# Optimization experiments

Measured on AMD Instinct MI355X. Metric: run time of the kernel, lower is better.

The kernel has to match this reference:

```python
import jax, jax.numpy as jnp
import numpy as np

# Detect.__init__ defaults from the source
TOP_K = 5000
CONF_THRESH = 0.01
NMS_THRESH = 0.3
VAR0, VAR1 = 0.1, 0.2   # variance = [0.1, 0.2]
NUM_CLASSES = 2

B = 16
IMAGE = 1280
FMAPS = [320, 160, 80, 40, 20, 10]          # image / steps [4,8,16,32,64,128]
MIN_SIZES = [16, 32, 64, 128, 256, 512]
AR = 1.5                                     # aspect_ratios = [[1.5]] * 6


def make_priors():
    """Vectorized PriorBox.forward: 1 prior per location (max_sizes=[], single AR)."""
    chunks = []
    for f, ms in zip(FMAPS, MIN_SIZES):
        c = (np.arange(f, dtype=np.float32) + 0.5) / f
        cy, cx = np.meshgrid(c, c, indexing='ij')
        s = ms / float(IMAGE)
        w = np.full_like(cx, s / np.sqrt(AR))   # s_k / sqrt(ar)
        h = np.full_like(cx, s * np.sqrt(AR))   # s_k * sqrt(ar)
        chunks.append(np.stack([cx, cy, w, h], -1).reshape(-1, 4))
    pr = np.concatenate(chunks, 0).clip(0.0, 1.0)   # clip=True
    return jnp.asarray(pr, jnp.float32)             # [136500, 4]


def setup_inputs() -> dict:
    key = jax.random.key(0)
    k1, k2 = jax.random.split(key)
    P = sum(f * f for f in FMAPS)   # 136500
    loc_data = 0.5 * jax.random.normal(k1, (B, P, 4), jnp.float32)
    conf_data = jax.random.uniform(k2, (B * P, NUM_CLASSES), jnp.float32)  # post-softmax probs
    prior_data = make_priors()
    return {"loc_data": loc_data, "conf_data": conf_data, "prior_data": prior_data}


def _decode(loc, priors):
    # SSD box decode with variances [0.1, 0.2]; loc, priors: [P,4]
    cxcy = priors[:, :2] + loc[:, :2] * VAR0 * priors[:, 2:]
    wh = priors[:, 2:] * jnp.exp(loc[:, 2:] * VAR1)
    xy1 = cxcy - wh * 0.5
    xy2 = xy1 + wh
    return jnp.concatenate([xy1, xy2], axis=-1)   # [P,4] x1y1x2y2


def _greedy_keep(boxes, valid):
    # Greedy NMS over score-sorted candidates. boxes [K,4], valid [K] bool.
    # Indices/keep decisions are discrete -> computed on stop_gradient'd boxes.
    b = jax.lax.stop_gradient(boxes)
    x1, y1, x2, y2 = b[:, 0], b[:, 1], b[:, 2], b[:, 3]
    area = (x2 - x1) * (y2 - y1)
    idxs = jnp.arange(b.shape[0])

    def body(keep, i):
        iw = jnp.maximum(jnp.minimum(x2, x2[i]) - jnp.maximum(x1, x1[i]), 0.0)
        ih = jnp.maximum(jnp.minimum(y2, y2[i]) - jnp.maximum(y1, y1[i]), 0.0)
        inter = iw * ih
        iou = inter / (area + area[i] - inter)
        suppress = keep[i] & (iou > NMS_THRESH) & (idxs > i)
        return keep & ~suppress, None

    keep, _ = jax.lax.scan(body, valid, idxs)
    return keep


def _detect_one(loc_i, conf_cl, priors):
    # loc_i [P,4]; conf_cl [P] = class-1 scores; returns [TOP_K, 5] (score, x1,y1,x2,y2)
    boxes = _decode(loc_i, priors)
    masked = jnp.where(conf_cl > CONF_THRESH, conf_cl, -1.0)   # c_mask gating
    order = jnp.argsort(-jax.lax.stop_gradient(masked))[:TOP_K]  # scores.sort, top_k cap
    s = masked[order]
    b = boxes[order]
    valid = s > CONF_THRESH
    keep = _greedy_keep(b, valid)
    # scatter kept (score, box) rows, in descending-score order, into dense output
    rank = jnp.cumsum(keep) - 1
    row = jnp.where(keep, rank, TOP_K)            # dropped rows -> scratch slot
    vals = jnp.concatenate([s[:, None], b], axis=1)
    vals = jnp.where(keep[:, None], vals, 0.0)
    out = jnp.zeros((TOP_K + 1, 5), jnp.float32).at[row].set(vals)
    return out[:TOP_K]


def reference(loc_data, conf_data, prior_data):
    num = loc_data.shape[0]
    P = prior_data.shape[0]
    conf_preds = conf_data.reshape(num, P, NUM_CLASSES).transpose(0, 2, 1)  # [B,2,P]
    cls1 = jax.vmap(_detect_one, in_axes=(0, 0, None))(loc_data, conf_preds[:, 1, :], prior_data)
    bg = jnp.zeros_like(cls1)                     # background class row stays zero
    output = jnp.stack([bg, cls1], axis=1)        # [B, 2, TOP_K, 5]
    # NOTE: the original's final `flt[(rank < top_k)...].fill_(0)` fills a boolean-indexed
    # COPY in torch, so it is a no-op on `output`; we faithfully return output unchanged.
    return output
```

## Files before the change

kernel.cpp:

```cpp
#include <hip/hip_runtime.h>
#include <math.h>

#pragma clang fp contract(off)

#define PNUM 136500
#define HPNUM 68250
#define BNUM 16
#define TOPK 5000
#define CAP 8192
#define NB2 1024
#define B2BASE 0xBC00u
#define NWORDS 79
#define NW32 158
#define GSTRIDE 32
#define CAPE 65536
#define ELDS 10240
#define NXB 128
#define BSTRIDE 5120
#define EBUF 3072

#define OFF_SC    ((size_t)0)
#define OFF_X1    (OFF_SC + 320000)
#define OFF_Y1    (OFF_X1 + 320000)
#define OFF_X2    (OFF_Y1 + 320000)
#define OFF_Y2    (OFF_X2 + 320000)
#define OFF_AREA  (OFF_Y2 + 320000)
#define OFF_HIST  ((size_t)1920000)
#define OFF_CUT   (OFF_HIST + 65536)
#define OFF_SBASE (OFF_CUT + 64)
#define OFF_GBCUR (OFF_SBASE + 65536)
#define OFF_KEYS  (OFF_GBCUR + 1048576)
#define OFF_ECNT  (OFF_KEYS + 1048576)
#define OFF_EDGE  (OFF_ECNT + 2048)
#define OFF_GRP   (OFF_EDGE + 4194304)
#define OFF_BOFS  (OFF_GRP)
#define OFF_SIDX  (OFF_GRP + 16384)
#define OFF_SBX1  (OFF_SIDX + 327680)
#define OFF_SBX2  (OFF_SBX1 + 327680)
#define OFF_SBY1  (OFF_SBX2 + 327680)
#define OFF_SBY2  (OFF_SBY1 + 327680)
#define OFF_SBAR  (OFF_SBY2 + 327680)

__device__ __forceinline__ unsigned f2ord(float f) {
    unsigned u = __float_as_uint(f);
    return (u & 0x80000000u) ? ~u : (u | 0x80000000u);
}
__device__ __forceinline__ float ord2f(unsigned o) {
    unsigned u = (o & 0x80000000u) ? (o ^ 0x80000000u) : ~o;
    return __uint_as_float(u);
}
__device__ __forceinline__ int bucketOf(float x) {
    int b = (int)((x + 0.6f) * 71.111115f);
    return (b < 0) ? 0 : ((b > 127) ? 127 : b);
}

__global__ void __launch_bounds__(256) k_hist(const float* __restrict__ conf,
                                              unsigned* __restrict__ hist) {
    __shared__ unsigned lh[NB2];
    int img = blockIdx.y;
    for (int i = threadIdx.x; i < NB2; i += 256) lh[i] = 0;
    __syncthreads();
    const float4* src = (const float4*)(conf + (size_t)img * PNUM * 2);
    int stride = gridDim.x * 256;
    for (int q = blockIdx.x * 256 + threadIdx.x; q < HPNUM; q += stride) {
        float4 v = src[q];
        if (v.y > 0.01f) atomicAdd(&lh[(f2ord(v.y) >> 16) - B2BASE], 1u);
        if (v.w > 0.01f) atomicAdd(&lh[(f2ord(v.w) >> 16) - B2BASE], 1u);
    }
    __syncthreads();
    unsigned* h = hist + (size_t)img * NB2;
    for (int i = threadIdx.x; i < NB2; i += 256) {
        unsigned c = lh[i];
        if (c) atomicAdd(&h[i], c);
    }
}

__global__ void __launch_bounds__(256) k_cutoff2(const unsigned* __restrict__ hist,
                                                 unsigned* __restrict__ cut,
                                                 unsigned* __restrict__ sbase) {
    __shared__ unsigned csum[256], suf[256];
    int img = blockIdx.x;
    int t = threadIdx.x;
    const unsigned* h = hist + (size_t)img * NB2;
    unsigned h0 = h[t * 4], h1 = h[t * 4 + 1], h2 = h[t * 4 + 2], h3 = h[t * 4 + 3];
    csum[t] = h0 + h1 + h2 + h3;
    __syncthreads();
    if (t == 0) {
        unsigned a = 0;
        for (int g = 255; g >= 0; --g) { unsigned c = csum[g]; suf[g] = a; a += c; }
        unsigned acc = 0, before = 0;
        int c = -1;
        for (int cc = 255; cc >= 0; --cc) {
            if (acc + csum[cc] >= (unsigned)TOPK) { c = cc; before = acc; break; }
            acc += csum[cc];
        }
        unsigned cutb = B2BASE;
        if (c >= 0) {
            unsigned s2 = before;
            cutb = B2BASE + (unsigned)c * 4u;
            for (int b = c * 4 + 3; b >= c * 4; --b) {
                s2 += h[b];
                if (s2 >= (unsigned)TOPK) { cutb = B2BASE + (unsigned)b; break; }
            }
        }
        cut[img] = cutb;
    }
    __syncthreads();
    unsigned a = suf[t];
    unsigned* sb = sbase + (size_t)img * NB2 + t * 4;
    sb[3] = a;
    sb[2] = a + h3;
    sb[1] = a + h3 + h2;
    sb[0] = a + h3 + h2 + h1;
}

__global__ void __launch_bounds__(256) k_gather2(
        const float* __restrict__ conf, const unsigned* __restrict__ cut,
        const unsigned* __restrict__ sbase, unsigned* __restrict__ gbcur,
        unsigned long long* __restrict__ keys) {
    int q = blockIdx.x * 256 + threadIdx.x;
    int img = blockIdx.y;
    if (q >= HPNUM) return;
    unsigned cutb = cut[img];
    float4 v = ((const float4*)(conf + (size_t)img * PNUM * 2))[q];
    const unsigned* sb = sbase + (size_t)img * NB2;
    unsigned* gc = gbcur + (size_t)img * NB2 * 16;
    unsigned long long* kp = keys + (size_t)img * CAP;
    #pragma unroll
    for (int e = 0; e < 2; ++e) {
        float s = e ? v.w : v.y;
        if (s > 0.01f) {
            unsigned o = f2ord(s);
            if ((o >> 16) >= cutb) {
                unsigned wb = (o >> 16) - B2BASE;
                unsigned pos = sb[wb] + atomicAdd(&gc[wb * 16], 1u);
                if (pos < (unsigned)CAP)
                    kp[pos] = ((unsigned long long)o << 32)
                              | (unsigned)(~(unsigned)(2 * q + e));
            }
        }
    }
}

__global__ void __launch_bounds__(256) k_ssort(
        unsigned long long* __restrict__ keys, const unsigned* __restrict__ hist,
        const unsigned* __restrict__ cut, const unsigned* __restrict__ sbase) {
    int img = blockIdx.y;
    int b = blockIdx.x;
    if (B2BASE + (unsigned)b < cut[img]) return;
    unsigned cnt = hist[(size_t)img * NB2 + b];
    if (cnt <= 1) return;
    if (cnt > 1024) cnt = 1024;
    unsigned base = sbase[(size_t)img * NB2 + b];
    __shared__ unsigned long long sk[1024];
    unsigned long long* kp = keys + (size_t)img * CAP + base;
    int tid = threadIdx.x;
    for (int i = tid; i < 1024; i += 256) sk[i] = (i < (int)cnt) ? kp[i] : 0ull;
    __syncthreads();
    for (int k = 2; k <= 1024; k <<= 1) {
        for (int j = k >> 1; j > 0; j >>= 1) {
            for (int t = tid; t < 512; t += 256) {
                int i = ((t & ~(j - 1)) << 1) | (t & (j - 1));
                int p = i | j;
                bool desc = ((i & k) == 0);
                unsigned long long a = sk[i], bb = sk[p];
                bool sw = desc ? (a < bb) : (a > bb);
                if (sw) { sk[i] = bb; sk[p] = a; }
            }
            __syncthreads();
        }
    }
    for (int i = tid; i < (int)cnt; i += 256) kp[i] = sk[i];
}

__global__ void __launch_bounds__(256) k_decode(
        const unsigned long long* __restrict__ keys,
        const float* __restrict__ loc, const float* __restrict__ pri,
        float* __restrict__ SC, float* __restrict__ X1, float* __restrict__ Y1,
        float* __restrict__ X2, float* __restrict__ Y2, float* __restrict__ AREA) {
    int gidx = blockIdx.x * 256 + threadIdx.x;
    if (gidx >= BNUM * TOPK) return;
    int img = gidx / TOPK;
    int r = gidx - img * TOPK;
    unsigned long long key = keys[(size_t)img * CAP + r];
    size_t o = (size_t)img * TOPK + r;
    if (key != 0ull) {
        unsigned ordv = (unsigned)(key >> 32);
        float s = ord2f(ordv);
        unsigned p = ~(unsigned)(key & 0xFFFFFFFFull);
        const float* lp = loc + ((size_t)img * PNUM + p) * 4;
        const float* pp = pri + (size_t)p * 4;
        float lx = lp[0], ly = lp[1], lw = lp[2], lh = lp[3];
        float px = pp[0], py = pp[1], pw = pp[2], ph = pp[3];
        float cx = px + (lx * 0.1f) * pw;
        float cy = py + (ly * 0.1f) * ph;
        float w = pw * expf(lw * 0.2f);
        float h = ph * expf(lh * 0.2f);
        float x1 = cx - w * 0.5f;
        float y1 = cy - h * 0.5f;
        float x2 = x1 + w;
        float y2 = y1 + h;
        SC[o] = s; X1[o] = x1; Y1[o] = y1; X2[o] = x2; Y2[o] = y2;
        AREA[o] = (x2 - x1) * (y2 - y1);
    } else {
        SC[o] = -1.0f; X1[o] = 0.f; Y1[o] = 0.f; X2[o] = 0.f; Y2[o] = 0.f;
        AREA[o] = 0.f;
    }
}

__global__ void __launch_bounds__(256) k_bucket(
        const float* __restrict__ X1, const float* __restrict__ X2,
        const float* __restrict__ Y1, const float* __restrict__ Y2,
        const float* __restrict__ AREA,
        unsigned* __restrict__ bofs, unsigned* __restrict__ sidx,
        float* __restrict__ sbx1, float* __restrict__ sbx2,
        float* __restrict__ sby1, float* __restrict__ sby2,
        float* __restrict__ sbar) {
    __shared__ unsigned bcnt[NXB], bpre[NXB + 1], bcur[NXB];
    int img = blockIdx.x;
    int tid = threadIdx.x;
    if (tid < NXB) bcnt[tid] = 0;
    __syncthreads();
    size_t ib = (size_t)img * TOPK;
    for (int r = tid; r < TOPK; r += 256)
        atomicAdd(&bcnt[bucketOf(X1[ib + r])], 1u);
    __syncthreads();
    if (tid == 0) {
        unsigned a = 0;
        for (int b = 0; b < NXB; ++b) { bpre[b] = a; a += bcnt[b]; }
        bpre[NXB] = a;
    }
    __syncthreads();
    if (tid < NXB) bcur[tid] = bpre[tid];
    if (tid <= NXB) bofs[img * 130 + tid] = bpre[tid];
    __syncthreads();
    int base = img * BSTRIDE;
    for (int r = tid; r < TOPK; r += 256) {
        float x = X1[ib + r];
        unsigned s = atomicAdd(&bcur[bucketOf(x)], 1u);
        sidx[base + s] = (unsigned)r;
        sbx1[base + s] = x;
        sbx2[base + s] = X2[ib + r];
        sby1[base + s] = Y1[ib + r];
        sby2[base + s] = Y2[ib + r];
        sbar[base + s] = AREA[ib + r];
    }
}

__global__ void __launch_bounds__(256) k_pair4(
        const unsigned* __restrict__ bofs, const unsigned* __restrict__ sidx,
        const float* __restrict__ sbx1, const float* __restrict__ sbx2,
        const float* __restrict__ sby1, const float* __restrict__ sby2,
        const float* __restrict__ sbar,
        unsigned* __restrict__ ecnt, unsigned* __restrict__ edges) {
    __shared__ unsigned ebuf[EBUF];
    __shared__ unsigned ecl, ebase;
    int img = blockIdx.y;
    int wid = threadIdx.x >> 6;
    int lane = threadIdx.x & 63;
    int sb0 = (blockIdx.x * 4 + wid) * 4;
    if (threadIdx.x == 0) ecl = 0;
    __syncthreads();
    unsigned* ec = ecnt + (size_t)img * GSTRIDE;
    unsigned* eg = edges + (size_t)img * CAPE;
    if (sb0 < TOPK) {
        int base = img * BSTRIDE;
        float x1k[4], x2k[4], y1k[4], y2k[4], ark[4];
        unsigned rk[4];
        bool act[4];
        #pragma unroll
        for (int k = 0; k < 4; ++k) {
            act[k] = (sb0 + k) < TOPK;
            int s = act[k] ? (sb0 + k) : sb0;
            x1k[k] = sbx1[base + s]; x2k[k] = sbx2[base + s];
            y1k[k] = sby1[base + s]; y2k[k] = sby2[base + s];
            ark[k] = sbar[base + s]; rk[k] = sidx[base + s];
        }
        int b1 = bucketOf(x1k[0]);
        int b2m = bucketOf(x2k[0]);
        #pragma unroll
        for (int k = 1; k < 4; ++k)
            if (act[k]) { int b = bucketOf(x2k[k]); if (b > b2m) b2m = b; }
        const unsigned* bo = bofs + img * 130;
        unsigned s0 = bo[b1], s1 = bo[b2m + 1];
        for (unsigned sb = s0 + lane; ; sb += 64) {
            bool in = (sb < s1);
            float bx1 = 0.f, bx2 = 0.f, by1 = 0.f, by2 = 0.f, bar = 0.f;
            unsigned r2 = 0;
            if (in) {
                bx1 = sbx1[base + sb]; bx2 = sbx2[base + sb];
                by1 = sby1[base + sb]; by2 = sby2[base + sb];
                bar = sbar[base + sb]; r2 = sidx[base + sb];
            }
            #pragma unroll
            for (int k = 0; k < 4; ++k) {
                bool hit = false;
                unsigned edge = 0;
                if (in && act[k] && bx1 >= x1k[k]
                    && !(bx1 == x1k[k] && r2 <= rk[k])) {
                    float dx = fminf(x2k[k], bx2) - fmaxf(x1k[k], bx1);
                    if (dx > 0.0f) {
                        float dy = fminf(y2k[k], by2) - fmaxf(y1k[k], by1);
                        if (dy > 0.0f) {
                            float inter = dx * dy;
                            float iou = inter / (bar + ark[k] - inter);
                            if (iou > 0.3f) {
                                unsigned su = (rk[k] < r2) ? rk[k] : r2;
                                unsigned vi = (rk[k] < r2) ? r2 : rk[k];
                                edge = (vi << 13) | su;
                                hit = true;
                            }
                        }
                    }
                }
                unsigned long long bal = __ballot(hit);
                if (bal) {
                    int n = __popcll(bal);
                    unsigned wb = 0;
                    if (lane == 0) wb = atomicAdd(&ecl, (unsigned)n);
                    wb = __shfl(wb, 0, 64);
                    if (hit) {
                        unsigned long long lt =
                            (lane == 0) ? 0ull : ((1ull << lane) - 1ull);
                        unsigned p = wb + (unsigned)__popcll(bal & lt);
                        if (p < (unsigned)EBUF) ebuf[p] = edge;
                        else {
                            unsigned gp = atomicAdd(ec, 1u);
                            if (gp < (unsigned)CAPE) eg[gp] = edge;
                        }
                    }
                }
            }
            if (sb - lane + 64 >= s1) break;
        }
    }
    __syncthreads();
    unsigned n = min(ecl, (unsigned)EBUF);
    if (threadIdx.x == 0 && n) ebase = atomicAdd(ec, n);
    __syncthreads();
    for (unsigned i = threadIdx.x; i < n; i += 256) {
        unsigned p = ebase + i;
        if (p < (unsigned)CAPE) eg[p] = ebuf[i];
    }
}

__global__ void __launch_bounds__(256) k_nms3(
        const float* __restrict__ SC, const float* __restrict__ X1,
        const float* __restrict__ Y1, const float* __restrict__ X2,
        const float* __restrict__ Y2,
        const unsigned* __restrict__ ecnt, const unsigned* __restrict__ edges,
        float* __restrict__ out) {
    __shared__ unsigned lgrp[ELDS];
    __shared__ unsigned undL[160], keptL[160], blockL[160];
    __shared__ unsigned pfx[80];
    __shared__ int chg[2];
    int img = blockIdx.x;
    int tid = threadIdx.x;
    int l = tid & 63;
    int wid = tid >> 6;
    size_t ib = (size_t)img * TOPK;
    const float* sc = SC + ib;

    if (tid < 160) { keptL[tid] = 0u; blockL[tid] = 0u; }
    if (tid < 2) chg[tid] = 0;
    for (int w = wid; w < NWORDS; w += 4) {
        int row = w * 64 + l;
        bool valid = (row < TOPK) && (sc[row] > 0.01f);
        unsigned long long b = __ballot(valid);
        if (l == 0) {
            undL[2 * w]     = (unsigned)b;
            undL[2 * w + 1] = (unsigned)(b >> 32);
        }
    }
    unsigned E = min(ecnt[(size_t)img * GSTRIDE], (unsigned)CAPE);
    const unsigned* eimg = edges + (size_t)img * CAPE;
    bool inl = (E <= (unsigned)ELDS);
    if (inl) for (unsigned e = tid; e < E; e += 256) lgrp[e] = eimg[e];
    __syncthreads();

    for (int round = 0; round < 256; ++round) {
        int par = round & 1;
        for (unsigned e = tid; e < E; e += 256) {
            unsigned ed = inl ? lgrp[e] : eimg[e];
            unsigned s = ed & 8191u;
            unsigned v = ed >> 13;
            unsigned sw = s >> 5, sb = s & 31u;
            unsigned vw = v >> 5, vb = 1u << (v & 31u);
            if ((keptL[sw] >> sb) & 1u) {
                if (undL[vw] & vb) {
                    unsigned old = atomicAnd(&undL[vw], ~vb);
                    if (old & vb) chg[par] = 1;
                }
            } else if ((undL[sw] >> sb) & 1u) {
                if (!(blockL[vw] & vb)) atomicOr(&blockL[vw], vb);
            }
        }
        __syncthreads();
        if (tid < NW32) {
            unsigned nk = undL[tid] & ~blockL[tid];
            if (nk) {
                keptL[tid] |= nk;
                undL[tid] &= ~nk;
                chg[par] = 1;
            }
            blockL[tid] = 0u;
        }
        if (tid == 0) chg[par ^ 1] = 0;
        __syncthreads();
        if (!chg[par]) break;
    }

    if (tid == 0) {
        unsigned acc = 0;
        for (int w = 0; w < NWORDS; ++w) {
            pfx[w] = acc;
            acc += (unsigned)(__popc(keptL[2 * w]) + __popc(keptL[2 * w + 1]));
        }
    }
    __syncthreads();
    const float* x1 = X1 + ib; const float* y1 = Y1 + ib;
    const float* x2 = X2 + ib; const float* y2 = Y2 + ib;
    float* op = out + (((size_t)img * 2) + 1) * TOPK * 5;
    for (int w = wid; w < NWORDS; w += 4) {
        unsigned long long kw =
            ((unsigned long long)keptL[2 * w + 1] << 32) | keptL[2 * w];
        if (!kw) continue;
        int row = w * 64 + l;
        if ((kw >> l) & 1ull) {
            int rank = (int)pfx[w] + (int)__popcll(kw & ((1ull << l) - 1ull));
            float* r = op + (size_t)rank * 5;
            r[0] = sc[row]; r[1] = x1[row]; r[2] = y1[row];
            r[3] = x2[row]; r[4] = y2[row];
        }
    }
}

extern "C" void kernel_launch(void* const* d_in, const int* in_sizes, int n_in,
                              void* d_out, int out_size, void* d_ws, size_t ws_size,
                              hipStream_t stream) {
    (void)in_sizes; (void)n_in; (void)ws_size;
    const float* loc  = (const float*)d_in[0];
    const float* conf = (const float*)d_in[1];
    const float* pri  = (const float*)d_in[2];
    float* out = (float*)d_out;
    char* ws = (char*)d_ws;

    float* SC   = (float*)(ws + OFF_SC);
    float* X1   = (float*)(ws + OFF_X1);
    float* Y1   = (float*)(ws + OFF_Y1);
    float* X2   = (float*)(ws + OFF_X2);
    float* Y2   = (float*)(ws + OFF_Y2);
    float* AREA = (float*)(ws + OFF_AREA);
    unsigned* hist = (unsigned*)(ws + OFF_HIST);
    unsigned* cut  = (unsigned*)(ws + OFF_CUT);
    unsigned* sbase = (unsigned*)(ws + OFF_SBASE);
    unsigned* gbcur = (unsigned*)(ws + OFF_GBCUR);
    unsigned long long* keys = (unsigned long long*)(ws + OFF_KEYS);
    unsigned* ecnt = (unsigned*)(ws + OFF_ECNT);
    unsigned* edges = (unsigned*)(ws + OFF_EDGE);
    unsigned* bofs = (unsigned*)(ws + OFF_BOFS);
    unsigned* sidx = (unsigned*)(ws + OFF_SIDX);
    float* sbx1 = (float*)(ws + OFF_SBX1);
    float* sbx2 = (float*)(ws + OFF_SBX2);
    float* sby1 = (float*)(ws + OFF_SBY1);
    float* sby2 = (float*)(ws + OFF_SBY2);
    float* sbar = (float*)(ws + OFF_SBAR);

    hipMemsetAsync(d_out, 0, (size_t)out_size * sizeof(float), stream);
    hipMemsetAsync(ws + OFF_HIST, 0, (OFF_ECNT + 2048) - OFF_HIST, stream);

    dim3 gh1(16, BNUM);
    k_hist<<<gh1, 256, 0, stream>>>(conf, hist);
    k_cutoff2<<<BNUM, 256, 0, stream>>>(hist, cut, sbase);
    dim3 gh2((HPNUM + 255) / 256, BNUM);
    k_gather2<<<gh2, 256, 0, stream>>>(conf, cut, sbase, gbcur, keys);
    dim3 gs(NB2, BNUM);
    k_ssort<<<gs, 256, 0, stream>>>(keys, hist, cut, sbase);
    k_decode<<<(BNUM * TOPK + 255) / 256, 256, 0, stream>>>(
        keys, loc, pri, SC, X1, Y1, X2, Y2, AREA);

    k_bucket<<<BNUM, 256, 0, stream>>>(X1, X2, Y1, Y2, AREA,
                                       bofs, sidx, sbx1, sbx2, sby1, sby2, sbar);
    dim3 pg((TOPK + 15) / 16, BNUM);
    k_pair4<<<pg, 256, 0, stream>>>(bofs, sidx, sbx1, sbx2, sby1, sby2, sbar,
                                    ecnt, edges);
    k_nms3<<<BNUM, 256, 0, stream>>>(SC, X1, Y1, X2, Y2, ecnt, edges, out);
}
```

Before: 255.0 us.

## Pack sorted boxes as float4, recompute areas, and prefetch candidates in pair kernel

Replaces the five separate sorted-coordinate arrays with one float4 array per box and recomputes box area on the fly instead of storing it, so each candidate needs one vector load instead of five scalar loads. The pair kernel's candidate loop now software-prefetches the next 64-wide chunk of boxes and indices while testing the current one. The area is computed the same way as before, so IoU results should match, at the cost of a few extra multiplies and more registers.

```diff
diff --git a/kernel.cpp b/kernel.cpp
--- a/kernel.cpp
+++ b/kernel.cpp
@@ -35,11 +35,7 @@
 #define OFF_GRP   (OFF_EDGE + 4194304)
 #define OFF_BOFS  (OFF_GRP)
 #define OFF_SIDX  (OFF_GRP + 16384)
-#define OFF_SBX1  (OFF_SIDX + 327680)
-#define OFF_SBX2  (OFF_SBX1 + 327680)
-#define OFF_SBY1  (OFF_SBX2 + 327680)
-#define OFF_SBY2  (OFF_SBY1 + 327680)
-#define OFF_SBAR  (OFF_SBY2 + 327680)
+#define OFF_SBOX  (OFF_SIDX + 327680)
 
 __device__ __forceinline__ unsigned f2ord(float f) {
     unsigned u = __float_as_uint(f);
@@ -177,7 +173,7 @@
         const unsigned long long* __restrict__ keys,
         const float* __restrict__ loc, const float* __restrict__ pri,
         float* __restrict__ SC, float* __restrict__ X1, float* __restrict__ Y1,
-        float* __restrict__ X2, float* __restrict__ Y2, float* __restrict__ AREA) {
+        float* __restrict__ X2, float* __restrict__ Y2) {
     int gidx = blockIdx.x * 256 + threadIdx.x;
     if (gidx >= BNUM * TOPK) return;
     int img = gidx / TOPK;
@@ -201,21 +197,16 @@
         float x2 = x1 + w;
         float y2 = y1 + h;
         SC[o] = s; X1[o] = x1; Y1[o] = y1; X2[o] = x2; Y2[o] = y2;
-        AREA[o] = (x2 - x1) * (y2 - y1);
     } else {
         SC[o] = -1.0f; X1[o] = 0.f; Y1[o] = 0.f; X2[o] = 0.f; Y2[o] = 0.f;
-        AREA[o] = 0.f;
     }
 }
 
 __global__ void __launch_bounds__(256) k_bucket(
         const float* __restrict__ X1, const float* __restrict__ X2,
         const float* __restrict__ Y1, const float* __restrict__ Y2,
-        const float* __restrict__ AREA,
         unsigned* __restrict__ bofs, unsigned* __restrict__ sidx,
-        float* __restrict__ sbx1, float* __restrict__ sbx2,
-        float* __restrict__ sby1, float* __restrict__ sby2,
-        float* __restrict__ sbar) {
+        float4* __restrict__ sbox) {
     __shared__ unsigned bcnt[NXB], bpre[NXB + 1], bcur[NXB];
     int img = blockIdx.x;
     int tid = threadIdx.x;
@@ -239,19 +230,13 @@
         float x = X1[ib + r];
         unsigned s = atomicAdd(&bcur[bucketOf(x)], 1u);
         sidx[base + s] = (unsigned)r;
-        sbx1[base + s] = x;
-        sbx2[base + s] = X2[ib + r];
-        sby1[base + s] = Y1[ib + r];
-        sby2[base + s] = Y2[ib + r];
-        sbar[base + s] = AREA[ib + r];
+        sbox[base + s] = make_float4(x, Y1[ib + r], X2[ib + r], Y2[ib + r]);
     }
 }
 
 __global__ void __launch_bounds__(256) k_pair4(
         const unsigned* __restrict__ bofs, const unsigned* __restrict__ sidx,
-        const float* __restrict__ sbx1, const float* __restrict__ sbx2,
-        const float* __restrict__ sby1, const float* __restrict__ sby2,
-        const float* __restrict__ sbar,
+        const float4* __restrict__ sbox,
         unsigned* __restrict__ ecnt, unsigned* __restrict__ edges) {
     __shared__ unsigned ebuf[EBUF];
     __shared__ unsigned ecl, ebase;
@@ -272,9 +257,10 @@
         for (int k = 0; k < 4; ++k) {
             act[k] = (sb0 + k) < TOPK;
             int s = act[k] ? (sb0 + k) : sb0;
-            x1k[k] = sbx1[base + s]; x2k[k] = sbx2[base + s];
-            y1k[k] = sby1[base + s]; y2k[k] = sby2[base + s];
-            ark[k] = sbar[base + s]; rk[k] = sidx[base + s];
+            float4 bk = sbox[base + s];
+            x1k[k] = bk.x; y1k[k] = bk.y; x2k[k] = bk.z; y2k[k] = bk.w;
+            ark[k] = (bk.z - bk.x) * (bk.w - bk.y);
+            rk[k] = sidx[base + s];
         }
         int b1 = bucketOf(x1k[0]);
         int b2m = bucketOf(x2k[0]);
@@ -283,55 +269,63 @@
             if (act[k]) { int b = bucketOf(x2k[k]); if (b > b2m) b2m = b; }
         const unsigned* bo = bofs + img * 130;
         unsigned s0 = bo[b1], s1 = bo[b2m + 1];
-        for (unsigned sb = s0 + lane; ; sb += 64) {
-            bool in = (sb < s1);
-            float bx1 = 0.f, bx2 = 0.f, by1 = 0.f, by2 = 0.f, bar = 0.f;
-            unsigned r2 = 0;
-            if (in) {
-                bx1 = sbx1[base + sb]; bx2 = sbx2[base + sb];
-                by1 = sby1[base + sb]; by2 = sby2[base + sb];
-                bar = sbar[base + sb]; r2 = sidx[base + sb];
-            }
-            #pragma unroll
-            for (int k = 0; k < 4; ++k) {
-                bool hit = false;
-                unsigned edge = 0;
-                if (in && act[k] && bx1 >= x1k[k]
-                    && !(bx1 == x1k[k] && r2 <= rk[k])) {
-                    float dx = fminf(x2k[k], bx2) - fmaxf(x1k[k], bx1);
-                    if (dx > 0.0f) {
-                        float dy = fminf(y2k[k], by2) - fmaxf(y1k[k], by1);
-                        if (dy > 0.0f) {
-                            float inter = dx * dy;
-                            float iou = inter / (bar + ark[k] - inter);
-                            if (iou > 0.3f) {
-                                unsigned su = (rk[k] < r2) ? rk[k] : r2;
-                                unsigned vi = (rk[k] < r2) ? r2 : rk[k];
-                                edge = (vi << 13) | su;
-                                hit = true;
+        if (s0 < s1) {
+            unsigned nit = (s1 - s0 + 63) >> 6;
+            unsigned c0 = s0 + (unsigned)lane;
+            if (c0 > s1 - 1) c0 = s1 - 1;
+            float4 cb = sbox[base + c0];
+            unsigned cr = sidx[base + c0];
+            for (unsigned it = 0; it < nit; ++it) {
+                float4 nb = cb; unsigned nr = cr;
+                if (it + 1 < nit) {
+                    unsigned cn = s0 + (it + 1) * 64 + (unsigned)lane;
+                    if (cn > s1 - 1) cn = s1 - 1;
+                    nb = sbox[base + cn];
+                    nr = sidx[base + cn];
+                }
+                bool in = (s0 + it * 64 + (unsigned)lane) < s1;
+                float bar = (cb.z - cb.x) * (cb.w - cb.y);
+                #pragma unroll
+                for (int k = 0; k < 4; ++k) {
+                    bool hit = false;
+                    unsigned edge = 0;
+                    if (in && act[k] && cb.x >= x1k[k]
+                        && !(cb.x == x1k[k] && cr <= rk[k])) {
+                        float dx = fminf(x2k[k], cb.z) - fmaxf(x1k[k], cb.x);
+                        if (dx > 0.0f) {
+                            float dy = fminf(y2k[k], cb.w) - fmaxf(y1k[k], cb.y);
+                            if (dy > 0.0f) {
+                                float inter = dx * dy;
+                                float iou = inter / (bar + ark[k] - inter);
+                                if (iou > 0.3f) {
+                                    unsigned su = (rk[k] < cr) ? rk[k] : cr;
+                                    unsigned vi = (rk[k] < cr) ? cr : rk[k];
+                                    edge = (vi << 13) | su;
+                                    hit = true;
+                                }
+                            }
+                        }
+                    }
+                    unsigned long long bal = __ballot(hit);
+                    if (bal) {
+                        int n = __popcll(bal);
+                        unsigned wb = 0;
+                        if (lane == 0) wb = atomicAdd(&ecl, (unsigned)n);
+                        wb = __shfl(wb, 0, 64);
+                        if (hit) {
+                            unsigned long long lt =
+                                (lane == 0) ? 0ull : ((1ull << lane) - 1ull);
+                            unsigned p = wb + (unsigned)__popcll(bal & lt);
+                            if (p < (unsigned)EBUF) ebuf[p] = edge;
+                            else {
+                                unsigned gp = atomicAdd(ec, 1u);
+                                if (gp < (unsigned)CAPE) eg[gp] = edge;
                             }
                         }
                     }
                 }
-                unsigned long long bal = __ballot(hit);
-                if (bal) {
-                    int n = __popcll(bal);
-                    unsigned wb = 0;
-                    if (lane == 0) wb = atomicAdd(&ecl, (unsigned)n);
-                    wb = __shfl(wb, 0, 64);
-                    if (hit) {
-                        unsigned long long lt =
-                            (lane == 0) ? 0ull : ((1ull << lane) - 1ull);
-                        unsigned p = wb + (unsigned)__popcll(bal & lt);
-                        if (p < (unsigned)EBUF) ebuf[p] = edge;
-                        else {
-                            unsigned gp = atomicAdd(ec, 1u);
-                            if (gp < (unsigned)CAPE) eg[gp] = edge;
-                        }
-                    }
-                }
-            }
-            if (sb - lane + 64 >= s1) break;
+                cb = nb; cr = nr;
+            }
         }
     }
     __syncthreads();
@@ -450,7 +444,6 @@
     float* Y1   = (float*)(ws + OFF_Y1);
     float* X2   = (float*)(ws + OFF_X2);
     float* Y2   = (float*)(ws + OFF_Y2);
-    float* AREA = (float*)(ws + OFF_AREA);
     unsigned* hist = (unsigned*)(ws + OFF_HIST);
     unsigned* cut  = (unsigned*)(ws + OFF_CUT);
     unsigned* sbase = (unsigned*)(ws + OFF_SBASE);
@@ -460,11 +453,7 @@
     unsigned* edges = (unsigned*)(ws + OFF_EDGE);
     unsigned* bofs = (unsigned*)(ws + OFF_BOFS);
     unsigned* sidx = (unsigned*)(ws + OFF_SIDX);
-    float* sbx1 = (float*)(ws + OFF_SBX1);
-    float* sbx2 = (float*)(ws + OFF_SBX2);
-    float* sby1 = (float*)(ws + OFF_SBY1);
-    float* sby2 = (float*)(ws + OFF_SBY2);
-    float* sbar = (float*)(ws + OFF_SBAR);
+    float4* sbox = (float4*)(ws + OFF_SBOX);
 
     hipMemsetAsync(d_out, 0, (size_t)out_size * sizeof(float), stream);
     hipMemsetAsync(ws + OFF_HIST, 0, (OFF_ECNT + 2048) - OFF_HIST, stream);
@@ -477,12 +466,10 @@
     dim3 gs(NB2, BNUM);
     k_ssort<<<gs, 256, 0, stream>>>(keys, hist, cut, sbase);
     k_decode<<<(BNUM * TOPK + 255) / 256, 256, 0, stream>>>(
-        keys, loc, pri, SC, X1, Y1, X2, Y2, AREA);
-
-    k_bucket<<<BNUM, 256, 0, stream>>>(X1, X2, Y1, Y2, AREA,
-                                       bofs, sidx, sbx1, sbx2, sby1, sby2, sbar);
+        keys, loc, pri, SC, X1, Y1, X2, Y2);
+
+    k_bucket<<<BNUM, 256, 0, stream>>>(X1, X2, Y1, Y2, bofs, sidx, sbox);
     dim3 pg((TOPK + 15) / 16, BNUM);
-    k_pair4<<<pg, 256, 0, stream>>>(bofs, sidx, sbx1, sbx2, sby1, sby2, sbar,
-                                    ecnt, edges);
+    k_pair4<<<pg, 256, 0, stream>>>(bofs, sidx, sbox, ecnt, edges);
     k_nms3<<<BNUM, 256, 0, stream>>>(SC, X1, Y1, X2, Y2, ecnt, edges, out);
 }
```

After: 243.9 us. -4.3%, faster.
